# Optimization experiments

Measured on AMD Instinct MI355X. Metric: run time of the kernel, lower is better.

The kernel has to match this reference:

```python
import jax, jax.numpy as jnp
import numpy as np

HIDDEN, NHEAD, NLAYERS = 128, 8, 4
N, H, W = 1, 36, 192


def _layernorm(x, w, b, eps=1e-5):
    mu = x.mean(-1, keepdims=True)
    var = ((x - mu) ** 2).mean(-1, keepdims=True)
    return (x - mu) * jax.lax.rsqrt(var + eps) * w + b


def _mha_rel(q_in, k_in, v_in, in_w, in_b, out_w, out_b, pos_sel, attn_mask):
    # q_in/k_in/v_in: [w, bsz, C]; pos_sel: [w, w, C] (already gathered by pos_indexes)
    w, bsz, C = q_in.shape
    hd = C // NHEAD
    scale = float(hd) ** -0.5
    wq, wk, wv = in_w[:C], in_w[C:2 * C], in_w[2 * C:]
    bq, bk, bv = in_b[:C], in_b[C:2 * C], in_b[2 * C:]
    q = (q_in @ wq.T + bq) * scale
    k = k_in @ wk.T + bk
    v = v_in @ wv.T + bv
    q_r = (pos_sel @ wq.T + bq) * scale            # [w,w,C]
    k_r = pos_sel @ wk.T + bk                       # [w,w,C]
    q = q.reshape(w, bsz, NHEAD, hd)
    k = k.reshape(w, bsz, NHEAD, hd)
    v = v.reshape(w, bsz, NHEAD, hd)
    q_r = q_r.reshape(w, w, NHEAD, hd)
    k_r = k_r.reshape(w, w, NHEAD, hd)
    # content-content + content-pos + pos-content -> [bsz, heads, w, w]
    attn = (jnp.einsum('wnec,vnec->newv', q, k)
            + jnp.einsum('wnec,wvec->newv', q, k_r)
            + jnp.einsum('vnec,wvec->newv', k, q_r))
    if attn_mask is not None:
        attn = attn + attn_mask[None, None]
    raw = attn
    a = jax.nn.softmax(attn, axis=-1)
    vo = jnp.einsum('newv,vnec->wnec', a, v).reshape(w, bsz, C)
    vo = vo @ out_w.T + out_b
    return vo, raw.sum(axis=1)  # raw summed over heads, [bsz,w,w]


def setup_inputs():
    key = jax.random.key(0)
    ks = jax.random.split(key, 8)
    C, L = HIDDEN, NLAYERS
    s = 0.02
    rn = lambda k, shape, sc: jax.random.normal(k, shape, dtype=jnp.float32) * sc
    return dict(
        feat_left=rn(ks[0], (N, C, H, W), 1.0),
        feat_right=rn(ks[1], (N, C, H, W), 1.0),
        pos_enc=rn(ks[2], (2 * W - 1, C), 1.0),
        sa_in_w=rn(ks[3], (L, 3 * C, C), s),
        sa_in_b=jnp.zeros((L, 3 * C), jnp.float32),
        sa_out_w=rn(ks[4], (L, C, C), s),
        sa_out_b=jnp.zeros((L, C), jnp.float32),
        sa_ln_w=jnp.ones((L, C), jnp.float32),
        sa_ln_b=jnp.zeros((L, C), jnp.float32),
        ca_in_w=rn(ks[5], (L, 3 * C, C), s),
        ca_in_b=jnp.zeros((L, 3 * C), jnp.float32),
        ca_out_w=rn(ks[6], (L, C, C), s),
        ca_out_b=jnp.zeros((L, C), jnp.float32),
        ca_ln1_w=jnp.ones((L, C), jnp.float32),
        ca_ln1_b=jnp.zeros((L, C), jnp.float32),
        ca_ln2_w=jnp.ones((L, C), jnp.float32),
        ca_ln2_b=jnp.zeros((L, C), jnp.float32),
    )


def reference(feat_left, feat_right, pos_enc,
              sa_in_w, sa_in_b, sa_out_w, sa_out_b, sa_ln_w, sa_ln_b,
              ca_in_w, ca_in_b, ca_out_w, ca_out_b,
              ca_ln1_w, ca_ln1_b, ca_ln2_w, ca_ln2_b):
    n, C, h, w = feat_left.shape
    hn = h * n
    # [N,C,H,W] -> [W,HN,C]
    fl = jnp.transpose(feat_left, (3, 2, 0, 1)).reshape(w, hn, C)
    fr = jnp.transpose(feat_right, (3, 2, 0, 1)).reshape(w, hn, C)
    # relative position indexes: (w-1..0) col + (0..w-1) row, flattened
    idx = (np.arange(w - 1, -1, -1)[:, None] + np.arange(w)[None, :]).reshape(-1)
    pos_sel = pos_enc[idx].reshape(w, w, C)             # for left-query attention
    pos_sel_flip = pos_enc[::-1][idx].reshape(w, w, C)  # flipped pos for right-query
    causal_mask = jnp.triu(jnp.full((w, w), -jnp.inf, dtype=jnp.float32), k=1)

    feat = jnp.concatenate([fl, fr], axis=1)  # [W, 2HN, C]
    raw_last = None
    for i in range(NLAYERS):
        # ---- self attention on concatenated tokens ----
        f2 = _layernorm(feat, sa_ln_w[i], sa_ln_b[i])
        vo, _ = _mha_rel(f2, f2, f2, sa_in_w[i], sa_in_b[i], sa_out_w[i], sa_out_b[i],
                         pos_sel, None)
        feat = feat + vo
        # ---- cross attention (shared weights for both directions) ----
        left, right = feat[:, :hn], feat[:, hn:]
        l2 = _layernorm(left, ca_ln1_w[i], ca_ln1_b[i])
        r2 = _layernorm(right, ca_ln1_w[i], ca_ln1_b[i])
        vo, _ = _mha_rel(r2, l2, l2, ca_in_w[i], ca_in_b[i], ca_out_w[i], ca_out_b[i],
                         pos_sel_flip, None)
        right = right + vo
        mask = causal_mask if i == NLAYERS - 1 else None
        r2b = _layernorm(right, ca_ln2_w[i], ca_ln2_b[i])
        vo, raw = _mha_rel(l2, r2b, r2b, ca_in_w[i], ca_in_b[i], ca_out_w[i], ca_out_b[i],
                           pos_sel, mask)
        left = left + vo
        feat = jnp.concatenate([left, right], axis=1)
        raw_last = raw
    # raw_last: [HN, W, W] -> [N, H, W, W]
    attn_weight = raw_last.reshape(h, n, w, w).transpose(1, 0, 2, 3)
    return attn_weight, feat
```

## Files before the change

kernel.cpp:

```cpp
#include <hip/hip_runtime.h>
#include <cmath>

#define W 192
#define CC 128
#define BSA 72
#define BCA 36
#define TSA (W*BSA)
#define TCA (W*BCA)
#define CH 32
#define SLD 200

__global__ __launch_bounds__(256) void pack_feat_k(const float* __restrict__ fl,
                                                   const float* __restrict__ fr,
                                                   float* __restrict__ feat) {
  __shared__ float tile[32][33];
  int b = blockIdx.z;
  const float* src = (b < BCA) ? fl : fr;
  int h = (b < BCA) ? b : b - BCA;
  int w0 = blockIdx.x * 32, c0 = blockIdx.y * 32;
  int tx = threadIdx.x & 31, ty = threadIdx.x >> 5;
#pragma unroll
  for (int rr = 0; rr < 4; ++rr) {
    int c = ty + rr * 8;
    tile[c][tx] = src[((c0 + c) * BCA + h) * W + w0 + tx];
  }
  __syncthreads();
#pragma unroll
  for (int rr = 0; rr < 4; ++rr) {
    int wl = ty + rr * 8;
    feat[(((w0 + wl) * BSA) + b) * CC + c0 + tx] = tile[tx][wl];
  }
}

__global__ __launch_bounds__(256) void copy_k(const float* __restrict__ src,
                                              float* __restrict__ dst, int n) {
  int i = blockIdx.x * 256 + threadIdx.x;
  if (i < n) dst[i] = src[i];
}

__global__ __launch_bounds__(256) void ln_k(const float* __restrict__ X,
                                            const float* __restrict__ g,
                                            const float* __restrict__ bta,
                                            float* __restrict__ Y,
                                            int T, int ob, int ooff) {
  int wv = threadIdx.x >> 6, lane = threadIdx.x & 63;
  int t = blockIdx.x * 4 + wv;
  if (t >= T) return;
  int srow = (t / ob) * BSA + (t % ob) + ooff;
  const float* x = X + srow * CC;
  float x0 = x[lane], x1 = x[lane + 64];
  float s = x0 + x1;
#pragma unroll
  for (int o = 32; o > 0; o >>= 1) s += __shfl_xor(s, o);
  float mu = s * (1.0f / CC);
  float d0 = x0 - mu, d1 = x1 - mu;
  float q = d0 * d0 + d1 * d1;
#pragma unroll
  for (int o = 32; o > 0; o >>= 1) q += __shfl_xor(q, o);
  float rstd = 1.0f / sqrtf(q * (1.0f / CC) + 1e-5f);
  Y[t * CC + lane] = d0 * rstd * g[lane] + bta[lane];
  Y[t * CC + lane + 64] = d1 * rstd * g[lane + 64] + bta[lane + 64];
}

__global__ __launch_bounds__(256) void ln_dual_k(const float* __restrict__ X,
                                                 const float* __restrict__ g,
                                                 const float* __restrict__ bta,
                                                 float* __restrict__ Y) {
  int wv = threadIdx.x >> 6, lane = threadIdx.x & 63;
  int t = blockIdx.x * 4 + wv;
  if (t >= 2 * TCA) return;
  int tt = (t >= TCA) ? t - TCA : t;
  int srow = (tt / 36) * BSA + (tt % 36) + ((t >= TCA) ? 36 : 0);
  const float* x = X + srow * CC;
  float x0 = x[lane], x1 = x[lane + 64];
  float s = x0 + x1;
#pragma unroll
  for (int o = 32; o > 0; o >>= 1) s += __shfl_xor(s, o);
  float mu = s * (1.0f / CC);
  float d0 = x0 - mu, d1 = x1 - mu;
  float q = d0 * d0 + d1 * d1;
#pragma unroll
  for (int o = 32; o > 0; o >>= 1) q += __shfl_xor(q, o);
  float rstd = 1.0f / sqrtf(q * (1.0f / CC) + 1e-5f);
  Y[t * CC + lane] = d0 * rstd * g[lane] + bta[lane];
  Y[t * CC + lane + 64] = d1 * rstd * g[lane + 64] + bta[lane + 64];
}

template<int TM>
__device__ __forceinline__ void gemm_core(
    const float* __restrict__ A, int lda,
    const float* __restrict__ Bw, int ldb,
    const float* __restrict__ bias,
    float* __restrict__ C, int ldc,
    int M, int N, int noff, int scale_abs, int accum, int ob, int ooff) {
  constexpr int MR = TM / 16;
  constexpr int AS = TM + 4;
  __shared__ float AsT[32 * AS];
  __shared__ float BsT[32 * 132];
  int tid = threadIdx.x;
  int ty = tid >> 4, tx = tid & 15;
  int t0 = blockIdx.x * TM, n0 = blockIdx.y * 128;
  float acc[MR][8] = {};
  for (int kc = 0; kc < 128; kc += 32) {
#pragma unroll
    for (int p = 0; p < TM / 32; ++p) {
      int id = tid + p * 256;
      int row = id >> 3, qk = id & 7;
      int arow = t0 + row;
      float4 av = make_float4(0.f, 0.f, 0.f, 0.f);
      if (arow < M) av = *reinterpret_cast<const float4*>(A + (long)arow * lda + kc + qk * 4);
      AsT[(qk * 4 + 0) * AS + row] = av.x;
      AsT[(qk * 4 + 1) * AS + row] = av.y;
      AsT[(qk * 4 + 2) * AS + row] = av.z;
      AsT[(qk * 4 + 3) * AS + row] = av.w;
    }
#pragma unroll
    for (int p = 0; p < 4; ++p) {
      int id = tid + p * 256;
      int row = id >> 3, qk = id & 7;
      int brow = n0 + row;
      float4 bv = make_float4(0.f, 0.f, 0.f, 0.f);
      if (brow < N) bv = *reinterpret_cast<const float4*>(Bw + (long)brow * ldb + kc + qk * 4);
      BsT[(qk * 4 + 0) * 132 + row] = bv.x;
      BsT[(qk * 4 + 1) * 132 + row] = bv.y;
      BsT[(qk * 4 + 2) * 132 + row] = bv.z;
      BsT[(qk * 4 + 3) * 132 + row] = bv.w;
    }
    __syncthreads();
#pragma unroll
    for (int k = 0; k < 32; ++k) {
      float a[MR];
      if constexpr (MR == 2) {
        float2 a0 = *reinterpret_cast<const float2*>(&AsT[k * AS + ty * 2]);
        a[0] = a0.x; a[1] = a0.y;
      } else if constexpr (MR == 4) {
        float4 a0 = *reinterpret_cast<const float4*>(&AsT[k * AS + ty * 4]);
        a[0] = a0.x; a[1] = a0.y; a[2] = a0.z; a[3] = a0.w;
      } else {
        float4 a0 = *reinterpret_cast<const float4*>(&AsT[k * AS + ty * 8]);
        float4 a1 = *reinterpret_cast<const float4*>(&AsT[k * AS + ty * 8 + 4]);
        a[0] = a0.x; a[1] = a0.y; a[2] = a0.z; a[3] = a0.w;
        a[4] = a1.x; a[5] = a1.y; a[6] = a1.z; a[7] = a1.w;
      }
      float4 b0 = *reinterpret_cast<const float4*>(&BsT[k * 132 + tx * 8]);
      float4 b1 = *reinterpret_cast<const float4*>(&BsT[k * 132 + tx * 8 + 4]);
      float bb[8] = {b0.x, b0.y, b0.z, b0.w, b1.x, b1.y, b1.z, b1.w};
#pragma unroll
      for (int i2 = 0; i2 < MR; ++i2)
#pragma unroll
        for (int j2 = 0; j2 < 8; ++j2)
          acc[i2][j2] += a[i2] * bb[j2];
    }
    __syncthreads();
  }
#pragma unroll
  for (int i2 = 0; i2 < MR; ++i2) {
    int t = t0 + ty * MR + i2;
    if (t >= M) continue;
    int orow = ob ? ((t / ob) * BSA + (t % ob) + ooff) : t;
    float* crow = C + (long)orow * ldc + noff;
#pragma unroll
    for (int j2 = 0; j2 < 8; ++j2) {
      int n = n0 + tx * 8 + j2;
      if (n >= N) continue;
      float val = acc[i2][j2] + (bias ? bias[n] : 0.f);
      if (noff + n < scale_abs) val *= 0.25f;
      if (accum) crow[n] += val; else crow[n] = val;
    }
  }
}

template<int TM>
__global__ __launch_bounds__(256) void gemm_g(
    const float* __restrict__ A, int lda, long abatch,
    const float* __restrict__ Bw, int ldb, long bbatch,
    const float* __restrict__ bias, int bzoff,
    float* __restrict__ C, int ldc, long cbatch,
    int M, int N, int noff, int nzoff, int scale_abs, int accum, int ob, int ooff) {
  int z = blockIdx.z;
  gemm_core<TM>(A + z * abatch, lda, Bw + z * bbatch, ldb,
                bias ? bias + z * bzoff : nullptr,
                C + z * cbatch, ldc, M, N, noff + z * nzoff,
                scale_abs, accum, ob, ooff);
}

__global__ __launch_bounds__(256) void ca_qkv_k(
    const float* __restrict__ Aq, const float* __restrict__ Akv,
    const float* __restrict__ w3, const float* __restrict__ b3,
    float* __restrict__ out) {
  int z = blockIdx.z;
  const float* A = (z == 0) ? Aq : Akv;
  gemm_core<32>(A, 128, w3 + z * 16384, 128, b3 + z * 128,
                out, 384, TCA, 128, z * 128, 128, 0, 0, 0);
}

__global__ __launch_bounds__(256) void pos_all_k(
    const float* __restrict__ pos,
    const float* __restrict__ saw, const float* __restrict__ sab,
    const float* __restrict__ caw, const float* __restrict__ cab,
    float* __restrict__ out) {
  int z = blockIdx.z;
  int layer = z >> 2, kind = z & 3;
  const float* w = ((kind < 2) ? saw : caw) + layer * 49152 + (kind & 1) * 16384;
  const float* b = ((kind < 2) ? sab : cab) + layer * 384 + (kind & 1) * 128;
  int sc = (kind & 1) ? 0 : 128;
  gemm_core<32>(pos, 128, w, 128, b, out + (long)z * 49152, 128,
                383, 128, 0, sc, 0, 0, 0);
}

__global__ __launch_bounds__(384) void attn_k(const float* __restrict__ qkv,
                                              const float* __restrict__ qpos,
                                              const float* __restrict__ kpos,
                                              float* __restrict__ vo,
                                              int B, int flip, int domask) {
  __shared__ float q_s[CH * 20];
  __shared__ float v_s[192 * 17];
  __shared__ float u_s[2 * 223 * 20];
  __shared__ float part[384];
  __shared__ float red_m[CH], red_il[CH];
  float* kp_s = u_s;
  float* qp_s = u_s + 223 * 20;
  float* S = u_s;

  int t = threadIdx.x;
  int col = (t >= 192) ? t - 192 : t;
  int rbase = (t >= 192) ? 16 : 0;
  int b = blockIdx.z, e = blockIdx.y, w0 = blockIdx.x * CH;

  for (int idx = t; idx < 192 * 4; idx += 384) {
    int row = idx >> 2, q4 = idx & 3;
    float4 kv = *reinterpret_cast<const float4*>(qkv + ((long)row * B + b) * 384 + 128 + e * 16 + q4 * 4);
    v_s[row * 17 + q4 * 4 + 0] = kv.x; v_s[row * 17 + q4 * 4 + 1] = kv.y;
    v_s[row * 17 + q4 * 4 + 2] = kv.z; v_s[row * 17 + q4 * 4 + 3] = kv.w;
  }
  __syncthreads();
  float kr[16];
#pragma unroll
  for (int d = 0; d < 16; ++d) kr[d] = v_s[col * 17 + d];
  __syncthreads();
  for (int idx = t; idx < 192 * 4; idx += 384) {
    int row = idx >> 2, q4 = idx & 3;
    float4 vv = *reinterpret_cast<const float4*>(qkv + ((long)row * B + b) * 384 + 256 + e * 16 + q4 * 4);
    v_s[row * 17 + q4 * 4 + 0] = vv.x; v_s[row * 17 + q4 * 4 + 1] = vv.y;
    v_s[row * 17 + q4 * 4 + 2] = vv.z; v_s[row * 17 + q4 * 4 + 3] = vv.w;
  }
  if (t < CH * 4) {
    int row = t >> 2, q4 = t & 3;
    float4 qv = *reinterpret_cast<const float4*>(qkv + ((long)(w0 + row) * B + b) * 384 + e * 16 + q4 * 4);
    *reinterpret_cast<float4*>(q_s + row * 20 + q4 * 4) = qv;
  }
  int base = flip ? w0 : (191 - (w0 + CH - 1));
  for (int idx = t; idx < 223 * 4; idx += 384) {
    int row = idx >> 2, q4 = idx & 3;
    int gidx = base + row;
    float4 kpv = make_float4(0.f, 0.f, 0.f, 0.f), qpv = kpv;
    if (gidx >= 0 && gidx < 383) {
      kpv = *reinterpret_cast<const float4*>(kpos + (long)gidx * 128 + e * 16 + q4 * 4);
      qpv = *reinterpret_cast<const float4*>(qpos + (long)gidx * 128 + e * 16 + q4 * 4);
    }
    *reinterpret_cast<float4*>(kp_s + row * 20 + q4 * 4) = kpv;
    *reinterpret_cast<float4*>(qp_s + row * 20 + q4 * 4) = qpv;
  }
  __syncthreads();

  float s[16];
#pragma unroll
  for (int rr = 0; rr < 16; ++rr) {
    int r = rbase + rr;
    int j = flip ? (191 + r - col) : (CH - 1 - r + col);
    const float4* kp4 = reinterpret_cast<const float4*>(kp_s + j * 20);
    const float4* qp4 = reinterpret_cast<const float4*>(qp_s + j * 20);
    const float4* qq4 = reinterpret_cast<const float4*>(q_s + r * 20);
    float acc = 0.f;
#pragma unroll
    for (int d4 = 0; d4 < 4; ++d4) {
      float4 kp = kp4[d4], qp = qp4[d4], qq = qq4[d4];
      acc += qq.x * (kr[d4 * 4 + 0] + kp.x) + kr[d4 * 4 + 0] * qp.x;
      acc += qq.y * (kr[d4 * 4 + 1] + kp.y) + kr[d4 * 4 + 1] * qp.y;
      acc += qq.z * (kr[d4 * 4 + 2] + kp.z) + kr[d4 * 4 + 2] * qp.z;
      acc += qq.w * (kr[d4 * 4 + 3] + kp.w) + kr[d4 * 4 + 3] * qp.w;
    }
    s[rr] = (domask && col > w0 + r) ? -INFINITY : acc;
  }
  __syncthreads();

#pragma unroll
  for (int rr = 0; rr < 16; ++rr) S[(rbase + rr) * SLD + col] = s[rr];
  __syncthreads();

  int r12 = t / 12, tr = t - r12 * 12;
  {
    float mloc = -INFINITY;
#pragma unroll
    for (int i = 0; i < 16; ++i) mloc = fmaxf(mloc, S[r12 * SLD + tr + 12 * i]);
    part[r12 * 12 + tr] = mloc;
  }
  __syncthreads();
  if (t < CH) {
    float m = part[t * 12];
#pragma unroll
    for (int i = 1; i < 12; ++i) m = fmaxf(m, part[t * 12 + i]);
    red_m[t] = m;
  }
  __syncthreads();
  {
    float m = red_m[r12];
    float lloc = 0.f;
#pragma unroll
    for (int i = 0; i < 16; ++i) {
      int a = r12 * SLD + tr + 12 * i;
      float p = __expf(S[a] - m);
      S[a] = p;
      lloc += p;
    }
    part[r12 * 12 + tr] = lloc;
  }
  __syncthreads();
  if (t < CH) {
    float l = 0.f;
#pragma unroll
    for (int i = 0; i < 12; ++i) l += part[t * 12 + i];
    red_il[t] = 1.0f / l;
  }
  __syncthreads();

  int d = t & 15, g = t >> 4;
  int r0 = g, r1 = g + 24;
  float a0 = 0.f, a1 = 0.f;
#pragma unroll 8
  for (int v4 = 0; v4 < 48; ++v4) {
    float4 s0 = *reinterpret_cast<const float4*>(S + r0 * SLD + v4 * 4);
    float va = v_s[(v4 * 4 + 0) * 17 + d];
    float vb = v_s[(v4 * 4 + 1) * 17 + d];
    float vc = v_s[(v4 * 4 + 2) * 17 + d];
    float vd = v_s[(v4 * 4 + 3) * 17 + d];
    a0 += s0.x * va + s0.y * vb + s0.z * vc + s0.w * vd;
    if (g < 8) {
      float4 s1 = *reinterpret_cast<const float4*>(S + r1 * SLD + v4 * 4);
      a1 += s1.x * va + s1.y * vb + s1.z * vc + s1.w * vd;
    }
  }
  vo[((long)(w0 + r0) * B + b) * 128 + e * 16 + d] = a0 * red_il[r0];
  if (g < 8)
    vo[((long)(w0 + r1) * B + b) * 128 + e * 16 + d] = a1 * red_il[r1];
}

__global__ __launch_bounds__(256) void gather_k(const float* __restrict__ D,
                                                const float* __restrict__ E,
                                                float* __restrict__ out) {
  __shared__ float E_s[192][33];
  int b = blockIdx.y, w0 = blockIdx.x * 32;
  for (int idx = threadIdx.x; idx < 192 * 32; idx += 256) {
    int v = idx >> 5, j = idx & 31;
    int u = 160 + v - w0 + j;
    E_s[v][j] = (u >= 0 && u < 192) ? E[((long)v * BCA + b) * 192 + u] : 0.f;
  }
  __syncthreads();
  int lane = threadIdx.x & 63, wl = threadIdx.x >> 6;
#pragma unroll
  for (int i = 0; i < 8; ++i) {
    int w = w0 + wl * 8 + i;
    int j = w0 + 31 - w;
#pragma unroll
    for (int kv = 0; kv < 3; ++kv) {
      int v = lane + kv * 64;
      long o = ((long)b * W + w) * W + v;
      if (v > w) {
        out[o] = -1e30f;
      } else {
        out[o] = out[o] + D[((long)w * BCA + b) * 192 + 191 + v - w] + E_s[v][j];
      }
    }
  }
}

extern "C" void kernel_launch(void* const* d_in, const int* in_sizes, int n_in,
                              void* d_out, int out_size, void* d_ws, size_t ws_size,
                              hipStream_t stream) {
  (void)in_sizes; (void)n_in; (void)out_size; (void)ws_size;
  const float* feat_left  = (const float*)d_in[0];
  const float* feat_right = (const float*)d_in[1];
  const float* pos_enc    = (const float*)d_in[2];
  const float* sa_in_w    = (const float*)d_in[3];
  const float* sa_in_b    = (const float*)d_in[4];
  const float* sa_out_w   = (const float*)d_in[5];
  const float* sa_out_b   = (const float*)d_in[6];
  const float* sa_ln_w    = (const float*)d_in[7];
  const float* sa_ln_b    = (const float*)d_in[8];
  const float* ca_in_w    = (const float*)d_in[9];
  const float* ca_in_b    = (const float*)d_in[10];
  const float* ca_out_w   = (const float*)d_in[11];
  const float* ca_out_b   = (const float*)d_in[12];
  const float* ca_ln1_w   = (const float*)d_in[13];
  const float* ca_ln1_b   = (const float*)d_in[14];
  const float* ca_ln2_w   = (const float*)d_in[15];
  const float* ca_ln2_b   = (const float*)d_in[16];

  float* ws   = (float*)d_ws;
  float* feat = ws;
  float* x2   = feat + 1769472;
  float* l2   = x2 + 1769472;
  float* r2   = l2 + 884736;
  float* qkv  = r2 + 884736;
  float* vo   = qkv + 5308416;
  float* posA = vo + 1769472;
  float* Dbuf = qkv + 2654208;
  float* Ebuf = Dbuf + 1327104;

  float* raw_out  = (float*)d_out;
  float* feat_out = raw_out + 1327104;

  pack_feat_k<<<dim3(6, 4, 72), 256, 0, stream>>>(feat_left, feat_right, feat);
  pos_all_k<<<dim3(12, 1, 16), 256, 0, stream>>>(pos_enc, sa_in_w, sa_in_b, ca_in_w, ca_in_b, posA);

  for (int i = 0; i < 4; ++i) {
    const float* inw  = sa_in_w + i * 49152;
    const float* inb  = sa_in_b + i * 384;
    const float* outw = sa_out_w + i * 16384;
    const float* outb = sa_out_b + i * 128;
    const float* saQ = posA + (long)(i * 4 + 0) * 49152;
    const float* saK = posA + (long)(i * 4 + 1) * 49152;
    const float* caQ = posA + (long)(i * 4 + 2) * 49152;
    const float* caK = posA + (long)(i * 4 + 3) * 49152;
    ln_k<<<dim3(TSA / 4), 256, 0, stream>>>(feat, sa_ln_w + i * 128, sa_ln_b + i * 128, x2, TSA, 72, 0);
    gemm_g<64><<<dim3(216, 1, 3), 256, 0, stream>>>(x2, 128, 0, inw, 128, 16384, inb, 128,
                                                    qkv, 384, 0, TSA, 128, 0, 128, 128, 0, 0, 0);
    attn_k<<<dim3(6, 8, 72), 384, 0, stream>>>(qkv, saQ, saK, vo, 72, 0, 0);
    gemm_g<32><<<dim3(432, 1, 1), 256, 0, stream>>>(vo, 128, 0, outw, 128, 0, outb, 0,
                                                    feat, 128, 0, TSA, 128, 0, 0, 0, 1, 0, 0);

    const float* cinw  = ca_in_w + i * 49152;
    const float* cinb  = ca_in_b + i * 384;
    const float* coutw = ca_out_w + i * 16384;
    const float* coutb = ca_out_b + i * 128;
    ln_dual_k<<<dim3(2 * TCA / 4), 256, 0, stream>>>(feat, ca_ln1_w + i * 128, ca_ln1_b + i * 128, l2);
    ca_qkv_k<<<dim3(216, 1, 3), 256, 0, stream>>>(r2, l2, cinw, cinb, qkv);
    attn_k<<<dim3(6, 8, 36), 384, 0, stream>>>(qkv, caQ, caK, vo, 36, 1, 0);
    gemm_g<32><<<dim3(216, 1, 1), 256, 0, stream>>>(vo, 128, 0, coutw, 128, 0, coutb, 0,
                                                    feat, 128, 0, TCA, 128, 0, 0, 0, 1, 36, 36);
    ln_k<<<dim3(TCA / 4), 256, 0, stream>>>(feat, ca_ln2_w + i * 128, ca_ln2_b + i * 128, r2, TCA, 36, 36);
    ca_qkv_k<<<dim3(216, 1, 3), 256, 0, stream>>>(l2, r2, cinw, cinb, qkv);
    attn_k<<<dim3(6, 8, 36), 384, 0, stream>>>(qkv, caQ, caK, vo, 36, 0, (i == 3) ? 1 : 0);
    if (i == 3) {
      gemm_g<32><<<dim3(216, 2, 1), 256, 0, stream>>>(qkv, 384, 0, caK, 128, 0, nullptr, 0,
                                                      Dbuf, 192, 0, TCA, 192, 0, 0, 0, 0, 0, 0);
      gemm_g<32><<<dim3(216, 2, 1), 256, 0, stream>>>(qkv + 128, 384, 0, caQ, 128, 0, nullptr, 0,
                                                      Ebuf, 192, 0, TCA, 192, 0, 0, 0, 0, 0, 0);
      gemm_g<32><<<dim3(6, 2, 36), 256, 0, stream>>>(qkv, 13824, 384, qkv + 128, 13824, 384, nullptr, 0,
                                                     raw_out, 192, 36864, 192, 192, 0, 0, 0, 0, 0, 0);
      gather_k<<<dim3(6, 36), 256, 0, stream>>>(Dbuf, Ebuf, raw_out);
    }
    gemm_g<32><<<dim3(216, 1, 1), 256, 0, stream>>>(vo, 128, 0, coutw, 128, 0, coutb, 0,
                                                    feat, 128, 0, TCA, 128, 0, 0, 0, 1, 36, 0);
  }

  copy_k<<<dim3((1769472 + 255) / 256), 256, 0, stream>>>(feat, feat_out, 1769472);
}
```

Measured before the change: 1.637 ms.

## Fuse LayerNorm into QKV GEMM prologue and drop separate LN/copy kernels

Removes the standalone LayerNorm kernels and computes each row's mean and variance inside the QKV GEMM, reading feat directly with strided row mapping. The last layer's out-projection epilogues also write into feat_out, which removes the final copy kernel, and the two Dbuf/Ebuf GEMMs are batched into one launch via the z dimension. This saves launches and intermediate buffer round-trips. In exchange, each GEMM block redundantly recomputes LN for its rows across the three z slices, and it uses a one-pass variance formula.

```diff
diff --git a/kernel.cpp b/kernel.cpp
--- a/kernel.cpp
+++ b/kernel.cpp
@@ -32,66 +32,13 @@
   }
 }
 
-__global__ __launch_bounds__(256) void copy_k(const float* __restrict__ src,
-                                              float* __restrict__ dst, int n) {
-  int i = blockIdx.x * 256 + threadIdx.x;
-  if (i < n) dst[i] = src[i];
-}
-
-__global__ __launch_bounds__(256) void ln_k(const float* __restrict__ X,
-                                            const float* __restrict__ g,
-                                            const float* __restrict__ bta,
-                                            float* __restrict__ Y,
-                                            int T, int ob, int ooff) {
-  int wv = threadIdx.x >> 6, lane = threadIdx.x & 63;
-  int t = blockIdx.x * 4 + wv;
-  if (t >= T) return;
-  int srow = (t / ob) * BSA + (t % ob) + ooff;
-  const float* x = X + srow * CC;
-  float x0 = x[lane], x1 = x[lane + 64];
-  float s = x0 + x1;
-#pragma unroll
-  for (int o = 32; o > 0; o >>= 1) s += __shfl_xor(s, o);
-  float mu = s * (1.0f / CC);
-  float d0 = x0 - mu, d1 = x1 - mu;
-  float q = d0 * d0 + d1 * d1;
-#pragma unroll
-  for (int o = 32; o > 0; o >>= 1) q += __shfl_xor(q, o);
-  float rstd = 1.0f / sqrtf(q * (1.0f / CC) + 1e-5f);
-  Y[t * CC + lane] = d0 * rstd * g[lane] + bta[lane];
-  Y[t * CC + lane + 64] = d1 * rstd * g[lane + 64] + bta[lane + 64];
-}
-
-__global__ __launch_bounds__(256) void ln_dual_k(const float* __restrict__ X,
-                                                 const float* __restrict__ g,
-                                                 const float* __restrict__ bta,
-                                                 float* __restrict__ Y) {
-  int wv = threadIdx.x >> 6, lane = threadIdx.x & 63;
-  int t = blockIdx.x * 4 + wv;
-  if (t >= 2 * TCA) return;
-  int tt = (t >= TCA) ? t - TCA : t;
-  int srow = (tt / 36) * BSA + (tt % 36) + ((t >= TCA) ? 36 : 0);
-  const float* x = X + srow * CC;
-  float x0 = x[lane], x1 = x[lane + 64];
-  float s = x0 + x1;
-#pragma unroll
-  for (int o = 32; o > 0; o >>= 1) s += __shfl_xor(s, o);
-  float mu = s * (1.0f / CC);
-  float d0 = x0 - mu, d1 = x1 - mu;
-  float q = d0 * d0 + d1 * d1;
-#pragma unroll
-  for (int o = 32; o > 0; o >>= 1) q += __shfl_xor(q, o);
-  float rstd = 1.0f / sqrtf(q * (1.0f / CC) + 1e-5f);
-  Y[t * CC + lane] = d0 * rstd * g[lane] + bta[lane];
-  Y[t * CC + lane + 64] = d1 * rstd * g[lane + 64] + bta[lane + 64];
-}
-
-template<int TM>
+template<int TM, bool LNA>
 __device__ __forceinline__ void gemm_core(
-    const float* __restrict__ A, int lda,
+    const float* __restrict__ A, int lda, int aob, int aooff,
+    const float* __restrict__ lnw, const float* __restrict__ lnb,
     const float* __restrict__ Bw, int ldb,
     const float* __restrict__ bias,
-    float* __restrict__ C, int ldc,
+    float* __restrict__ C, float* __restrict__ Cb, int ldc,
     int M, int N, int noff, int scale_abs, int accum, int ob, int ooff) {
   constexpr int MR = TM / 16;
   constexpr int AS = TM + 4;
@@ -100,19 +47,63 @@
   int tid = threadIdx.x;
   int ty = tid >> 4, tx = tid & 15;
   int t0 = blockIdx.x * TM, n0 = blockIdx.y * 128;
+  int row_l = tid >> 3, qk7 = tid & 7;
   float acc[MR][8] = {};
-  for (int kc = 0; kc < 128; kc += 32) {
+
+  float4 va[TM / 32][4];
+  if constexpr (LNA) {
+    float4 gv[4], bvv[4];
+#pragma unroll
+    for (int c4 = 0; c4 < 4; ++c4) {
+      gv[c4]  = *reinterpret_cast<const float4*>(lnw + c4 * 32 + qk7 * 4);
+      bvv[c4] = *reinterpret_cast<const float4*>(lnb + c4 * 32 + qk7 * 4);
+    }
 #pragma unroll
     for (int p = 0; p < TM / 32; ++p) {
-      int id = tid + p * 256;
-      int row = id >> 3, qk = id & 7;
-      int arow = t0 + row;
-      float4 av = make_float4(0.f, 0.f, 0.f, 0.f);
-      if (arow < M) av = *reinterpret_cast<const float4*>(A + (long)arow * lda + kc + qk * 4);
-      AsT[(qk * 4 + 0) * AS + row] = av.x;
-      AsT[(qk * 4 + 1) * AS + row] = av.y;
-      AsT[(qk * 4 + 2) * AS + row] = av.z;
-      AsT[(qk * 4 + 3) * AS + row] = av.w;
+      int ar = t0 + row_l + p * 32;
+      if (ar >= M) ar = M - 1;
+      int sr = (ar / aob) * BSA + (ar % aob) + aooff;
+      const float* arow = A + (long)sr * lda;
+      float sum = 0.f, sq = 0.f;
+#pragma unroll
+      for (int c4 = 0; c4 < 4; ++c4) {
+        va[p][c4] = *reinterpret_cast<const float4*>(arow + c4 * 32 + qk7 * 4);
+        sum += va[p][c4].x + va[p][c4].y + va[p][c4].z + va[p][c4].w;
+        sq += va[p][c4].x * va[p][c4].x + va[p][c4].y * va[p][c4].y
+            + va[p][c4].z * va[p][c4].z + va[p][c4].w * va[p][c4].w;
+      }
+      sum += __shfl_xor(sum, 1); sum += __shfl_xor(sum, 2); sum += __shfl_xor(sum, 4);
+      sq  += __shfl_xor(sq, 1);  sq  += __shfl_xor(sq, 2);  sq  += __shfl_xor(sq, 4);
+      float mu = sum * (1.f / 128.f);
+      float var = sq * (1.f / 128.f) - mu * mu;
+      float rstd = 1.0f / sqrtf(var + 1e-5f);
+#pragma unroll
+      for (int c4 = 0; c4 < 4; ++c4) {
+        va[p][c4].x = (va[p][c4].x - mu) * rstd * gv[c4].x + bvv[c4].x;
+        va[p][c4].y = (va[p][c4].y - mu) * rstd * gv[c4].y + bvv[c4].y;
+        va[p][c4].z = (va[p][c4].z - mu) * rstd * gv[c4].z + bvv[c4].z;
+        va[p][c4].w = (va[p][c4].w - mu) * rstd * gv[c4].w + bvv[c4].w;
+      }
+    }
+  }
+
+  for (int kcc = 0; kcc < 4; ++kcc) {
+    int kc = kcc * 32;
+#pragma unroll
+    for (int p = 0; p < TM / 32; ++p) {
+      int row = row_l + p * 32;
+      float4 av;
+      if constexpr (LNA) {
+        av = va[p][kcc];
+      } else {
+        int arow = t0 + row;
+        av = make_float4(0.f, 0.f, 0.f, 0.f);
+        if (arow < M) av = *reinterpret_cast<const float4*>(A + (long)arow * lda + kc + qk7 * 4);
+      }
+      AsT[(qk7 * 4 + 0) * AS + row] = av.x;
+      AsT[(qk7 * 4 + 1) * AS + row] = av.y;
+      AsT[(qk7 * 4 + 2) * AS + row] = av.z;
+      AsT[(qk7 * 4 + 3) * AS + row] = av.w;
     }
 #pragma unroll
     for (int p = 0; p < 4; ++p) {
@@ -159,13 +150,16 @@
     if (t >= M) continue;
     int orow = ob ? ((t / ob) * BSA + (t % ob) + ooff) : t;
     float* crow = C + (long)orow * ldc + noff;
+    float* crow2 = Cb ? Cb + (long)orow * ldc + noff : nullptr;
 #pragma unroll
     for (int j2 = 0; j2 < 8; ++j2) {
       int n = n0 + tx * 8 + j2;
       if (n >= N) continue;
       float val = acc[i2][j2] + (bias ? bias[n] : 0.f);
       if (noff + n < scale_abs) val *= 0.25f;
-      if (accum) crow[n] += val; else crow[n] = val;
+      if (accum) val += crow[n];
+      crow[n] = val;
+      if (crow2) crow2[n] = val;
     }
   }
 }
@@ -175,23 +169,40 @@
     const float* __restrict__ A, int lda, long abatch,
     const float* __restrict__ Bw, int ldb, long bbatch,
     const float* __restrict__ bias, int bzoff,
-    float* __restrict__ C, int ldc, long cbatch,
+    float* __restrict__ C, float* __restrict__ Cb, int ldc, long cbatch,
     int M, int N, int noff, int nzoff, int scale_abs, int accum, int ob, int ooff) {
   int z = blockIdx.z;
-  gemm_core<TM>(A + z * abatch, lda, Bw + z * bbatch, ldb,
-                bias ? bias + z * bzoff : nullptr,
-                C + z * cbatch, ldc, M, N, noff + z * nzoff,
-                scale_abs, accum, ob, ooff);
-}
-
-__global__ __launch_bounds__(256) void ca_qkv_k(
-    const float* __restrict__ Aq, const float* __restrict__ Akv,
+  gemm_core<TM, false>(A + z * abatch, lda, 0, 0, nullptr, nullptr,
+                       Bw + z * bbatch, ldb,
+                       bias ? bias + z * bzoff : nullptr,
+                       C + z * cbatch, Cb, ldc, M, N, noff + z * nzoff,
+                       scale_abs, accum, ob, ooff);
+}
+
+__global__ __launch_bounds__(256) void sa_qkv_k(
+    const float* __restrict__ feat,
+    const float* __restrict__ lnw, const float* __restrict__ lnb,
     const float* __restrict__ w3, const float* __restrict__ b3,
     float* __restrict__ out) {
   int z = blockIdx.z;
-  const float* A = (z == 0) ? Aq : Akv;
-  gemm_core<32>(A, 128, w3 + z * 16384, 128, b3 + z * 128,
-                out, 384, TCA, 128, z * 128, 128, 0, 0, 0);
+  gemm_core<64, true>(feat, 128, 72, 0, lnw, lnb,
+                      w3 + z * 16384, 128, b3 + z * 128,
+                      out, nullptr, 384, TSA, 128, z * 128, 128, 0, 0, 0);
+}
+
+__global__ __launch_bounds__(256) void ca_qkv_k(
+    const float* __restrict__ feat,
+    const float* __restrict__ lnwA, const float* __restrict__ lnbA, int ooffA,
+    const float* __restrict__ lnwB, const float* __restrict__ lnbB, int ooffB,
+    const float* __restrict__ w3, const float* __restrict__ b3,
+    float* __restrict__ out) {
+  int z = blockIdx.z;
+  const float* lw = (z == 0) ? lnwA : lnwB;
+  const float* lb = (z == 0) ? lnbA : lnbB;
+  int aoo = (z == 0) ? ooffA : ooffB;
+  gemm_core<32, true>(feat, 128, 36, aoo, lw, lb,
+                      w3 + z * 16384, 128, b3 + z * 128,
+                      out, nullptr, 384, TCA, 128, z * 128, 128, 0, 0, 0);
 }
 
 __global__ __launch_bounds__(256) void pos_all_k(
@@ -204,8 +215,9 @@
   const float* w = ((kind < 2) ? saw : caw) + layer * 49152 + (kind & 1) * 16384;
   const float* b = ((kind < 2) ? sab : cab) + layer * 384 + (kind & 1) * 128;
   int sc = (kind & 1) ? 0 : 128;
-  gemm_core<32>(pos, 128, w, 128, b, out + (long)z * 49152, 128,
-                383, 128, 0, sc, 0, 0, 0);
+  gemm_core<32, false>(pos, 128, 0, 0, nullptr, nullptr, w, 128, b,
+                       out + (long)z * 49152, nullptr, 128,
+                       383, 128, 0, sc, 0, 0, 0);
 }
 
 __global__ __launch_bounds__(384) void attn_k(const float* __restrict__ qkv,
@@ -398,10 +410,7 @@
 
   float* ws   = (float*)d_ws;
   float* feat = ws;
-  float* x2   = feat + 1769472;
-  float* l2   = x2 + 1769472;
-  float* r2   = l2 + 884736;
-  float* qkv  = r2 + 884736;
+  float* qkv  = feat + 1769472;
   float* vo   = qkv + 5308416;
   float* posA = vo + 1769472;
   float* Dbuf = qkv + 2654208;
@@ -422,37 +431,33 @@
     const float* saK = posA + (long)(i * 4 + 1) * 49152;
     const float* caQ = posA + (long)(i * 4 + 2) * 49152;
     const float* caK = posA + (long)(i * 4 + 3) * 49152;
-    ln_k<<<dim3(TSA / 4), 256, 0, stream>>>(feat, sa_ln_w + i * 128, sa_ln_b + i * 128, x2, TSA, 72, 0);
-    gemm_g<64><<<dim3(216, 1, 3), 256, 0, stream>>>(x2, 128, 0, inw, 128, 16384, inb, 128,
-                                                    qkv, 384, 0, TSA, 128, 0, 128, 128, 0, 0, 0);
+    const float* ln1w = ca_ln1_w + i * 128, *ln1b = ca_ln1_b + i * 128;
+    const float* ln2w = ca_ln2_w + i * 128, *ln2b = ca_ln2_b + i * 128;
+    float* fo = (i == 3) ? feat_out : nullptr;
+
+    sa_qkv_k<<<dim3(216, 1, 3), 256, 0, stream>>>(feat, sa_ln_w + i * 128, sa_ln_b + i * 128, inw, inb, qkv);
     attn_k<<<dim3(6, 8, 72), 384, 0, stream>>>(qkv, saQ, saK, vo, 72, 0, 0);
     gemm_g<32><<<dim3(432, 1, 1), 256, 0, stream>>>(vo, 128, 0, outw, 128, 0, outb, 0,
-                                                    feat, 128, 0, TSA, 128, 0, 0, 0, 1, 0, 0);
+                                                    feat, nullptr, 128, 0, TSA, 128, 0, 0, 0, 1, 0, 0);
 
     const float* cinw  = ca_in_w + i * 49152;
     const float* cinb  = ca_in_b + i * 384;
     const float* coutw = ca_out_w + i * 16384;
     const float* coutb = ca_out_b + i * 128;
-    ln_dual_k<<<dim3(2 * TCA / 4), 256, 0, stream>>>(feat, ca_ln1_w + i * 128, ca_ln1_b + i * 128, l2);
-    ca_qkv_k<<<dim3(216, 1, 3), 256, 0, stream>>>(r2, l2, cinw, cinb, qkv);
+    ca_qkv_k<<<dim3(216, 1, 3), 256, 0, stream>>>(feat, ln1w, ln1b, 36, ln1w, ln1b, 0, cinw, cinb, qkv);
     attn_k<<<dim3(6, 8, 36), 384, 0, stream>>>(qkv, caQ, caK, vo, 36, 1, 0);
     gemm_g<32><<<dim3(216, 1, 1), 256, 0, stream>>>(vo, 128, 0, coutw, 128, 0, coutb, 0,
-                                                    feat, 128, 0, TCA, 128, 0, 0, 0, 1, 36, 36);
-    ln_k<<<dim3(TCA / 4), 256, 0, stream>>>(feat, ca_ln2_w + i * 128, ca_ln2_b + i * 128, r2, TCA, 36, 36);
-    ca_qkv_k<<<dim3(216, 1, 3), 256, 0, stream>>>(l2, r2, cinw, cinb, qkv);
+                                                    feat, fo, 128, 0, TCA, 128, 0, 0, 0, 1, 36, 36);
+    ca_qkv_k<<<dim3(216, 1, 3), 256, 0, stream>>>(feat, ln1w, ln1b, 0, ln2w, ln2b, 36, cinw, cinb, qkv);
     attn_k<<<dim3(6, 8, 36), 384, 0, stream>>>(qkv, caQ, caK, vo, 36, 0, (i == 3) ? 1 : 0);
     if (i == 3) {
-      gemm_g<32><<<dim3(216, 2, 1), 256, 0, stream>>>(qkv, 384, 0, caK, 128, 0, nullptr, 0,
-                                                      Dbuf, 192, 0, TCA, 192, 0, 0, 0, 0, 0, 0);
-      gemm_g<32><<<dim3(216, 2, 1), 256, 0, stream>>>(qkv + 128, 384, 0, caQ, 128, 0, nullptr, 0,
-                                                      Ebuf, 192, 0, TCA, 192, 0, 0, 0, 0, 0, 0);
+      gemm_g<32><<<dim3(216, 2, 2), 256, 0, stream>>>(qkv, 384, 128, caK, 128, -49152, nullptr, 0,
+                                                      Dbuf, nullptr, 192, 1327104, TCA, 192, 0, 0, 0, 0, 0, 0);
       gemm_g<32><<<dim3(6, 2, 36), 256, 0, stream>>>(qkv, 13824, 384, qkv + 128, 13824, 384, nullptr, 0,
-                                                     raw_out, 192, 36864, 192, 192, 0, 0, 0, 0, 0, 0);
+                                                     raw_out, nullptr, 192, 36864, 192, 192, 0, 0, 0, 0, 0, 0);
       gather_k<<<dim3(6, 36), 256, 0, stream>>>(Dbuf, Ebuf, raw_out);
     }
     gemm_g<32><<<dim3(216, 1, 1), 256, 0, stream>>>(vo, 128, 0, coutw, 128, 0, coutb, 0,
-                                                    feat, 128, 0, TCA, 128, 0, 0, 0, 1, 36, 0);
-  }
-
-  copy_k<<<dim3((1769472 + 255) / 256), 256, 0, stream>>>(feat, feat_out, 1769472);
-}
+                                                    feat, fo, 128, 0, TCA, 128, 0, 0, 0, 1, 36, 0);
+  }
+}
```

Result: no change. 1.626 ms (-0.7%).
